# Optimization experiments

Hardware: AMD Instinct MI355X
Metric: run time of the kernel (lower is better)

## Reference

```python
import jax, jax.numpy as jnp
import numpy as np


def setup_inputs() -> dict:
    key = jax.random.key(0)
    k1, k2, k3, k4 = jax.random.split(key, 4)
    d_in, d_out = 1024, 1024
    x = jax.random.normal(k1, (4, 2048, d_in), dtype=jnp.float32)
    # nn.Linear weights, stored as [d_in, d_out] for x @ W (torch stores transpose)
    s = 1.0 / np.sqrt(d_in)
    Wq = jax.random.normal(k2, (d_in, d_out), dtype=jnp.float32) * s
    Wk = jax.random.normal(k3, (d_in, d_out), dtype=jnp.float32) * s
    Wv = jax.random.normal(k4, (d_in, d_out), dtype=jnp.float32) * s
    return {"x": x, "Wq": Wq, "Wk": Wk, "Wv": Wv}


def reference(x, Wq, Wk, Wv):
    # x: [b, s, d_in]; projections (no bias)
    q = jnp.einsum('bsi,io->bso', x, Wq)
    k = jnp.einsum('bsi,io->bso', x, Wk)
    v = jnp.einsum('bsi,io->bso', x, Wv)
    d_out = k.shape[-1]
    scores = jnp.einsum('bqd,bkd->bqk', q, k) / jnp.sqrt(jnp.float32(d_out))
    seq_len = x.shape[1]
    causal = jnp.tril(jnp.ones((seq_len, seq_len), dtype=bool))  # [s, s]
    scores = jnp.where(causal[None, :, :], scores, -jnp.inf)
    weights = jax.nn.softmax(scores, axis=-1)
    return jnp.einsum('bqk,bkd->bqd', weights, v)
```

## Files before the change

### kernel.cpp

```cpp
#include <hip/hip_runtime.h>

typedef __attribute__((ext_vector_type(8))) short bf16x8;
typedef __attribute__((ext_vector_type(4))) float f32x4;
typedef unsigned int u32;

__device__ __forceinline__ unsigned short f2bf(float f) {
  union { float f; unsigned int u; } a; a.f = f;
  unsigned int u = a.u;
  u += 0x7FFFu + ((u >> 16) & 1u);
  return (unsigned short)(u >> 16);
}
__device__ __forceinline__ float bf2f(unsigned short h) {
  union { unsigned int u; float f; } a; a.u = ((unsigned int)h) << 16;
  return a.f;
}

__device__ __forceinline__ void gload16(const unsigned short* g, unsigned short* l) {
  __builtin_amdgcn_global_load_lds((const __attribute__((address_space(1))) u32*)g,
                                   (__attribute__((address_space(3))) u32*)l, 16, 0, 0);
}

#define TM 128
#define TN 128
#define BK 64

template<int MODE>
__global__ __launch_bounds__(256, 4)
void gemm_bt(const unsigned short* __restrict__ A,
             const unsigned short* __restrict__ Bm,
             float* __restrict__ Cf,
             float* __restrict__ Cf2,
             unsigned short* __restrict__ Cb,
             int K, long aBatch, long bBatch, long cBatch, float scale)
{
  int z = blockIdx.z;
  A  += (long)z * aBatch;
  Bm += (long)z * bBatch;
  if (MODE == 2) { Cb += (long)z * cBatch; Cf += (long)z * 2048; }
  if (MODE == 3) { Cf += (long)z * cBatch; Cf2 += (long)z * 1024 * 1024; }

  int bm, bn, kStart = 0, kEnd;
  bool toMain = true;
  if (MODE == 2) {
    int f = blockIdx.x;
    int r = (int)((sqrtf((float)(8 * f + 1)) - 1.0f) * 0.5f);
    while ((r + 1) * (r + 2) / 2 <= f) r++;
    while (r * (r + 1) / 2 > f) r--;
    bm = r * TM;
    bn = (f - r * (r + 1) / 2) * TN;
    kEnd = K;
  } else if (MODE == 3) {
    int yy = blockIdx.y;
    if (yy < 16) {
      int s = 15 - yy;
      bm = s * TM;
      kEnd = (s < 8) ? 128 * (s + 1) : 64 * (s + 1);
    } else {
      int s = yy - 8;
      bm = s * TM;
      kStart = 64 * (s + 1);
      kEnd = 128 * (s + 1);
      toMain = false;
    }
    bn = blockIdx.x * TN;
  } else {
    bm = blockIdx.y * TM;
    bn = blockIdx.x * TN;
    kEnd = K;
  }

  __shared__ __align__(16) unsigned short As[TM * BK];
  __shared__ __align__(16) unsigned short Bs[TN * BK];

  int tid  = threadIdx.x;
  int wave = tid >> 6, lane = tid & 63;
  int wm = (wave >> 1) * 64, wn = (wave & 1) * 64;
  int quad = lane >> 4, l16 = lane & 15;

  int r8 = lane >> 3;
  int c  = (lane & 7) ^ r8;
  int rs = wave * 32 + r8;
  const unsigned short* Ag = A  + (long)(bm + rs) * K + c * 8;
  const unsigned short* Bg = Bm + (long)(bn + rs) * K + c * 8;
  unsigned short* Al = &As[(wave * 32) * BK];
  unsigned short* Bl = &Bs[(wave * 32) * BK];

  f32x4 acc[4][4] = {};

  for (int k0 = kStart; k0 < kEnd; k0 += BK) {
#pragma unroll
    for (int g = 0; g < 4; g++) {
      gload16(Ag + k0 + (long)g * 8 * K, Al + g * 8 * BK);
      gload16(Bg + k0 + (long)g * 8 * K, Bl + g * 8 * BK);
    }
    __syncthreads();

#pragma unroll
    for (int h = 0; h < 2; h++) {
      bf16x8 af[4], bfr[4];
#pragma unroll
      for (int i = 0; i < 4; i++)
        af[i]  = *(const bf16x8*)&As[(wm + i * 16 + l16) * BK + (((quad + 4 * h) ^ (l16 & 7)) * 8)];
#pragma unroll
      for (int j = 0; j < 4; j++)
        bfr[j] = *(const bf16x8*)&Bs[(wn + j * 16 + l16) * BK + (((quad + 4 * h) ^ (l16 & 7)) * 8)];
#pragma unroll
      for (int i = 0; i < 4; i++)
#pragma unroll
        for (int j = 0; j < 4; j++)
          acc[i][j] = __builtin_amdgcn_mfma_f32_16x16x32_bf16(af[i], bfr[j], acc[i][j], 0, 0, 0);
    }
    __syncthreads();
  }

#pragma unroll
  for (int i = 0; i < 4; i++) {
    int grow0 = bm + wm + i * 16 + quad * 4;
    if (MODE == 2) {
#pragma unroll
      for (int r = 0; r < 4; r++) {
        int grow = grow0 + r;
        float rowpart = 0.f;
#pragma unroll
        for (int j = 0; j < 4; j++) {
          int gcol = bn + wn + j * 16 + l16;
          float e = (gcol <= grow) ? __expf(acc[i][j][r] * scale) : 0.f;
          rowpart += e;
          Cb[(long)grow * 2048 + gcol] = f2bf(e);
        }
        rowpart += __shfl_xor(rowpart, 1);
        rowpart += __shfl_xor(rowpart, 2);
        rowpart += __shfl_xor(rowpart, 4);
        rowpart += __shfl_xor(rowpart, 8);
        if (l16 == 0) atomicAdd(&Cf[grow], rowpart);
      }
    } else {
#pragma unroll
      for (int j = 0; j < 4; j++) {
        int gcol = bn + wn + j * 16 + l16;
        if (MODE == 0) {
          int which = gcol >> 10;
          int col = gcol & 1023;
          if (which < 2) {
            unsigned short* dst = Cb + (long)which * 8192 * 1024;
#pragma unroll
            for (int r = 0; r < 4; r++)
              dst[(long)(grow0 + r) * 1024 + col] = f2bf(acc[i][j][r]);
          } else {
            unsigned short* Vt = Cb + (long)2 * 8192 * 1024;
            int bb = grow0 >> 11, s = grow0 & 2047;
            ushort4 pk;
            pk.x = f2bf(acc[i][j][0]); pk.y = f2bf(acc[i][j][1]);
            pk.z = f2bf(acc[i][j][2]); pk.w = f2bf(acc[i][j][3]);
            *(ushort4*)(Vt + ((long)bb * 1024 + col) * 2048 + s) = pk;
          }
        } else {
          if (toMain) {
#pragma unroll
            for (int r = 0; r < 4; r++)
              Cf[(long)(grow0 + r) * 1024 + gcol] = acc[i][j][r];
          } else {
#pragma unroll
            for (int r = 0; r < 4; r++)
              Cf2[(long)(grow0 + r - 1024) * 1024 + gcol] = acc[i][j][r];
          }
        }
      }
    }
  }
}

__global__ __launch_bounds__(256)
void cvt_bf16(const float* __restrict__ in, unsigned short* __restrict__ out, long n)
{
  long i = ((long)blockIdx.x * 256 + threadIdx.x) * 4;
  if (i >= n) return;
  float4 v = *(const float4*)(in + i);
  ushort4 o;
  o.x = f2bf(v.x); o.y = f2bf(v.y); o.z = f2bf(v.z); o.w = f2bf(v.w);
  *(ushort4*)(out + i) = o;
}

__global__ __launch_bounds__(256)
void zero_rsum(float* __restrict__ rsum)
{
  long i = ((long)blockIdx.x * 256 + threadIdx.x) * 4;
  float4 zz = {0.f, 0.f, 0.f, 0.f};
  *(float4*)(rsum + i) = zz;
}

__global__ __launch_bounds__(256)
void trans_cvt(const float* __restrict__ W0, const float* __restrict__ W1, const float* __restrict__ W2,
               unsigned short* __restrict__ T0, unsigned short* __restrict__ T1, unsigned short* __restrict__ T2)
{
  int z = blockIdx.z;
  const float* W   = (z == 0) ? W0 : (z == 1) ? W1 : W2;
  unsigned short* T = (z == 0) ? T0 : (z == 1) ? T1 : T2;
  __shared__ float tile[32][33];
  int kb = blockIdx.x * 32, nb = blockIdx.y * 32;
  int tx = threadIdx.x & 31, ty = threadIdx.x >> 5;
  for (int r = ty; r < 32; r += 8)
    tile[r][tx] = W[(long)(kb + r) * 1024 + nb + tx];
  __syncthreads();
  for (int r = ty; r < 32; r += 8)
    T[(long)(nb + r) * 1024 + kb + tx] = f2bf(tile[tx][r]);
}

__global__ __launch_bounds__(256)
void finalize(float* __restrict__ out, const float* __restrict__ O2,
              const float* __restrict__ rsum)
{
  int r = blockIdx.x, b = blockIdx.y;
  float rinv = 1.0f / rsum[(long)b * 2048 + r];
  long o = (((long)b * 2048 + r) * 1024) + threadIdx.x * 4;
  float4 v = *(const float4*)(out + o);
  if (r >= 1024) {
    long o2 = (((long)b * 1024 + (r - 1024)) * 1024) + threadIdx.x * 4;
    float4 w = *(const float4*)(O2 + o2);
    v.x += w.x; v.y += w.y; v.z += w.z; v.w += w.w;
  }
  v.x *= rinv; v.y *= rinv; v.z *= rinv; v.w *= rinv;
  *(float4*)(out + o) = v;
}

extern "C" void kernel_launch(void* const* d_in, const int* in_sizes, int n_in,
                              void* d_out, int out_size, void* d_ws, size_t ws_size,
                              hipStream_t stream) {
  const float* x  = (const float*)d_in[0];
  const float* Wq = (const float*)d_in[1];
  const float* Wk = (const float*)d_in[2];
  const float* Wv = (const float*)d_in[3];
  float* out = (float*)d_out;

  unsigned short* Xb  = (unsigned short*)d_ws;
  unsigned short* WqT = Xb  + (long)8192 * 1024;
  unsigned short* Q   = WqT + (long)3072 * 1024;
  unsigned short* Kb  = Q   + (long)8192 * 1024;
  unsigned short* Vt  = Kb  + (long)8192 * 1024;
  unsigned short* E   = Vt  + (long)8192 * 1024;
  float* O2           = (float*)(E + (long)4 * 2048 * 2048);
  float* rsum         = O2 + (long)4 * 1024 * 1024;
  unsigned short* WkT = WqT + (long)1024 * 1024;
  unsigned short* WvT = WkT + (long)1024 * 1024;

  cvt_bf16<<<8192, 256, 0, stream>>>(x, Xb, (long)8388608);
  trans_cvt<<<dim3(32, 32, 3), 256, 0, stream>>>(Wq, Wk, Wv, WqT, WkT, WvT);
  zero_rsum<<<8, 256, 0, stream>>>(rsum);

  gemm_bt<0><<<dim3(24, 64, 1), 256, 0, stream>>>(Xb, WqT, nullptr, nullptr, Q,
      1024, 0, 0, 0, 1.f);

  gemm_bt<2><<<dim3(136, 1, 4), 256, 0, stream>>>(Q, Kb, rsum, nullptr, E, 1024,
      (long)2048 * 1024, (long)2048 * 1024, (long)2048 * 2048, 0.03125f);

  gemm_bt<3><<<dim3(8, 24, 4), 256, 0, stream>>>(E, Vt, out, O2, nullptr, 2048,
      (long)2048 * 2048, (long)1024 * 2048, (long)2048 * 1024, 1.f);

  finalize<<<dim3(2048, 4), 256, 0, stream>>>(out, O2, rsum);
}
```

Before: 243.4 us.

## Fuse softmax normalization into PV GEMM epilogue and drop split-K

```diff
diff --git a/kernel.cpp b/kernel.cpp
--- a/kernel.cpp
+++ b/kernel.cpp
@@ -9,10 +9,6 @@
   unsigned int u = a.u;
   u += 0x7FFFu + ((u >> 16) & 1u);
   return (unsigned short)(u >> 16);
-}
-__device__ __forceinline__ float bf2f(unsigned short h) {
-  union { unsigned int u; float f; } a; a.u = ((unsigned int)h) << 16;
-  return a.f;
 }
 
 __device__ __forceinline__ void gload16(const unsigned short* g, unsigned short* l) {
@@ -37,10 +33,9 @@
   A  += (long)z * aBatch;
   Bm += (long)z * bBatch;
   if (MODE == 2) { Cb += (long)z * cBatch; Cf += (long)z * 2048; }
-  if (MODE == 3) { Cf += (long)z * cBatch; Cf2 += (long)z * 1024 * 1024; }
-
-  int bm, bn, kStart = 0, kEnd;
-  bool toMain = true;
+  if (MODE == 3) { Cf += (long)z * cBatch; Cf2 += (long)z * 2048; }
+
+  int bm, bn;
   if (MODE == 2) {
     int f = blockIdx.x;
     int r = (int)((sqrtf((float)(8 * f + 1)) - 1.0f) * 0.5f);
@@ -48,26 +43,14 @@
     while (r * (r + 1) / 2 > f) r--;
     bm = r * TM;
     bn = (f - r * (r + 1) / 2) * TN;
-    kEnd = K;
   } else if (MODE == 3) {
-    int yy = blockIdx.y;
-    if (yy < 16) {
-      int s = 15 - yy;
-      bm = s * TM;
-      kEnd = (s < 8) ? 128 * (s + 1) : 64 * (s + 1);
-    } else {
-      int s = yy - 8;
-      bm = s * TM;
-      kStart = 64 * (s + 1);
-      kEnd = 128 * (s + 1);
-      toMain = false;
-    }
+    bm = (15 - blockIdx.y) * TM;
     bn = blockIdx.x * TN;
   } else {
     bm = blockIdx.y * TM;
     bn = blockIdx.x * TN;
-    kEnd = K;
   }
+  int Keff = (MODE == 3) ? (bm + TM) : K;
 
   __shared__ __align__(16) unsigned short As[TM * BK];
   __shared__ __align__(16) unsigned short Bs[TN * BK];
@@ -87,7 +70,7 @@
 
   f32x4 acc[4][4] = {};
 
-  for (int k0 = kStart; k0 < kEnd; k0 += BK) {
+  for (int k0 = 0; k0 < Keff; k0 += BK) {
 #pragma unroll
     for (int g = 0; g < 4; g++) {
       gload16(Ag + k0 + (long)g * 8 * K, Al + g * 8 * BK);
@@ -134,36 +117,35 @@
         rowpart += __shfl_xor(rowpart, 8);
         if (l16 == 0) atomicAdd(&Cf[grow], rowpart);
       }
-    } else {
+    } else if (MODE == 3) {
+      float rinv[4];
+#pragma unroll
+      for (int r = 0; r < 4; r++) rinv[r] = 1.0f / Cf2[grow0 + r];
 #pragma unroll
       for (int j = 0; j < 4; j++) {
         int gcol = bn + wn + j * 16 + l16;
-        if (MODE == 0) {
-          int which = gcol >> 10;
-          int col = gcol & 1023;
-          if (which < 2) {
-            unsigned short* dst = Cb + (long)which * 8192 * 1024;
-#pragma unroll
-            for (int r = 0; r < 4; r++)
-              dst[(long)(grow0 + r) * 1024 + col] = f2bf(acc[i][j][r]);
-          } else {
-            unsigned short* Vt = Cb + (long)2 * 8192 * 1024;
-            int bb = grow0 >> 11, s = grow0 & 2047;
-            ushort4 pk;
-            pk.x = f2bf(acc[i][j][0]); pk.y = f2bf(acc[i][j][1]);
-            pk.z = f2bf(acc[i][j][2]); pk.w = f2bf(acc[i][j][3]);
-            *(ushort4*)(Vt + ((long)bb * 1024 + col) * 2048 + s) = pk;
-          }
+#pragma unroll
+        for (int r = 0; r < 4; r++)
+          Cf[(long)(grow0 + r) * 1024 + gcol] = acc[i][j][r] * rinv[r];
+      }
+    } else {
+#pragma unroll
+      for (int j = 0; j < 4; j++) {
+        int gcol = bn + wn + j * 16 + l16;
+        int which = gcol >> 10;
+        int col = gcol & 1023;
+        if (which < 2) {
+          unsigned short* dst = Cb + (long)which * 8192 * 1024;
+#pragma unroll
+          for (int r = 0; r < 4; r++)
+            dst[(long)(grow0 + r) * 1024 + col] = f2bf(acc[i][j][r]);
         } else {
-          if (toMain) {
-#pragma unroll
-            for (int r = 0; r < 4; r++)
-              Cf[(long)(grow0 + r) * 1024 + gcol] = acc[i][j][r];
-          } else {
-#pragma unroll
-            for (int r = 0; r < 4; r++)
-              Cf2[(long)(grow0 + r - 1024) * 1024 + gcol] = acc[i][j][r];
-          }
+          unsigned short* Vt = Cb + (long)2 * 8192 * 1024;
+          int bb = grow0 >> 11, s = grow0 & 2047;
+          ushort4 pk;
+          pk.x = f2bf(acc[i][j][0]); pk.y = f2bf(acc[i][j][1]);
+          pk.z = f2bf(acc[i][j][2]); pk.w = f2bf(acc[i][j][3]);
+          *(ushort4*)(Vt + ((long)bb * 1024 + col) * 2048 + s) = pk;
         }
       }
     }
@@ -206,23 +188,6 @@
     T[(long)(nb + r) * 1024 + kb + tx] = f2bf(tile[tx][r]);
 }
 
-__global__ __launch_bounds__(256)
-void finalize(float* __restrict__ out, const float* __restrict__ O2,
-              const float* __restrict__ rsum)
-{
-  int r = blockIdx.x, b = blockIdx.y;
-  float rinv = 1.0f / rsum[(long)b * 2048 + r];
-  long o = (((long)b * 2048 + r) * 1024) + threadIdx.x * 4;
-  float4 v = *(const float4*)(out + o);
-  if (r >= 1024) {
-    long o2 = (((long)b * 1024 + (r - 1024)) * 1024) + threadIdx.x * 4;
-    float4 w = *(const float4*)(O2 + o2);
-    v.x += w.x; v.y += w.y; v.z += w.z; v.w += w.w;
-  }
-  v.x *= rinv; v.y *= rinv; v.z *= rinv; v.w *= rinv;
-  *(float4*)(out + o) = v;
-}
-
 extern "C" void kernel_launch(void* const* d_in, const int* in_sizes, int n_in,
                               void* d_out, int out_size, void* d_ws, size_t ws_size,
                               hipStream_t stream) {
@@ -238,8 +203,7 @@
   unsigned short* Kb  = Q   + (long)8192 * 1024;
   unsigned short* Vt  = Kb  + (long)8192 * 1024;
   unsigned short* E   = Vt  + (long)8192 * 1024;
-  float* O2           = (float*)(E + (long)4 * 2048 * 2048);
-  float* rsum         = O2 + (long)4 * 1024 * 1024;
+  float* rsum         = (float*)(E + (long)4 * 2048 * 2048);
   unsigned short* WkT = WqT + (long)1024 * 1024;
   unsigned short* WvT = WkT + (long)1024 * 1024;
 
@@ -253,8 +217,6 @@
   gemm_bt<2><<<dim3(136, 1, 4), 256, 0, stream>>>(Q, Kb, rsum, nullptr, E, 1024,
       (long)2048 * 1024, (long)2048 * 1024, (long)2048 * 2048, 0.03125f);
 
-  gemm_bt<3><<<dim3(8, 24, 4), 256, 0, stream>>>(E, Vt, out, O2, nullptr, 2048,
+  gemm_bt<3><<<dim3(8, 16, 4), 256, 0, stream>>>(E, Vt, out, rsum, nullptr, 2048,
       (long)2048 * 2048, (long)1024 * 2048, (long)2048 * 1024, 1.f);
-
-  finalize<<<dim3(2048, 4), 256, 0, stream>>>(out, O2, rsum);
-}
+}
```

Result: no change. 239.0 us (-1.8%).
